# Performance work log

Hardware: AMD Instinct MI355X
Metric: run time of the kernel (lower is better)

The kernel has to match this reference:

```python
import jax, jax.numpy as jnp
import numpy as np

N_NODES = 100000


def _sage_conv(x, src, dst, W_l, W_r, b, num_nodes):
    # PyG SAGEConv with mean aggregation:
    # out_i = (mean_{j: (j->i) in E} x_j) @ W_l + x_i @ W_r + b
    msg_sum = jax.ops.segment_sum(x[src], dst, num_segments=num_nodes)  # [N, F]
    deg = jax.ops.segment_sum(jnp.ones_like(src, dtype=x.dtype), dst, num_segments=num_nodes)
    agg = msg_sum / jnp.maximum(deg, 1.0)[:, None]
    return agg @ W_l + x @ W_r + b


def setup_inputs() -> dict:
    key = jax.random.key(0)
    k = jax.random.split(key, 7)
    F_IN, H, C = 128, 128, 14
    E = 1600000
    x = jax.random.normal(k[0], (N_NODES, F_IN), dtype=jnp.float32)
    edge_index = jax.random.randint(k[1], (2, E), 0, N_NODES, dtype=jnp.int64)
    s = 1.0 / np.sqrt(F_IN)
    W1_l = jax.random.normal(k[2], (F_IN, H), dtype=jnp.float32) * s
    W1_r = jax.random.normal(k[3], (F_IN, H), dtype=jnp.float32) * s
    b1 = jnp.zeros((H,), dtype=jnp.float32)
    sh = 1.0 / np.sqrt(H)
    W2_l = jax.random.normal(k[4], (H, C), dtype=jnp.float32) * sh
    W2_r = jax.random.normal(k[5], (H, C), dtype=jnp.float32) * sh
    b2 = jnp.zeros((C,), dtype=jnp.float32)
    return {"x": x, "edge_index": edge_index, "edge_SF_num": 6,
            "W1_l": W1_l, "W1_r": W1_r, "b1": b1,
            "W2_l": W2_l, "W2_r": W2_r, "b2": b2}


def reference(x, edge_index, edge_SF_num, W1_l, W1_r, b1, W2_l, W2_r, b2):
    src, dst = edge_index[0], edge_index[1]
    h = _sage_conv(x, src, dst, W1_l, W1_r, b1, N_NODES)
    h = jax.nn.relu(h)
    # dropout is identity at inference (training=False)
    out = _sage_conv(h, src, dst, W2_l, W2_r, b2, N_NODES)
    x_SF = jax.nn.log_softmax(out[:, :edge_SF_num], axis=1)
    x_Ptx = jax.nn.log_softmax(out[:, edge_SF_num:], axis=1)
    return (x_SF, x_Ptx)
```

## Files before the change

kernel.cpp:

```cpp
#include <hip/hip_runtime.h>
#include <hip/hip_bf16.h>

#define NN 100000
#define F 128
#define C_OUT 14
#define ZP 16
#define WIN 64
#define NWIN ((NN + WIN - 1) / WIN)
#define WCAP 1408
#define EBATCH 4096
#define HS 136

typedef __attribute__((ext_vector_type(8))) short v8s;
typedef __attribute__((ext_vector_type(4))) float v4f;
typedef __attribute__((ext_vector_type(2))) float v2f;

static __device__ __forceinline__ unsigned short f2bf(float f) {
    unsigned int u = __float_as_uint(f);
    unsigned int r = (u + 0x7fffu + ((u >> 16) & 1u)) >> 16;
    return (unsigned short)r;
}
static __device__ __forceinline__ unsigned int pack2(float a, float b) {
    return (unsigned int)f2bf(a) | ((unsigned int)f2bf(b) << 16);
}
static __device__ __forceinline__ void unpack2(unsigned int u, float& lo, float& hi) {
    lo = __uint_as_float(u << 16);
    hi = __uint_as_float(u & 0xffff0000u);
}
static __device__ __forceinline__ void accf8(const uint2 u, float* a) {
    v2f f0 = __builtin_amdgcn_cvt_pk_f32_fp8((int)u.x, false);
    a[0] += f0[0]; a[1] += f0[1];
    v2f f1 = __builtin_amdgcn_cvt_pk_f32_fp8((int)u.x, true);
    a[2] += f1[0]; a[3] += f1[1];
    v2f f2 = __builtin_amdgcn_cvt_pk_f32_fp8((int)u.y, false);
    a[4] += f2[0]; a[5] += f2[1];
    v2f f3 = __builtin_amdgcn_cvt_pk_f32_fp8((int)u.y, true);
    a[6] += f3[0]; a[7] += f3[1];
}
static __device__ __forceinline__ unsigned int bf4_to_fp8x4(const unsigned short* sp) {
    float f0, f1, f2, f3;
    unpack2(*(const unsigned int*)(sp + 0), f0, f1);
    unpack2(*(const unsigned int*)(sp + 2), f2, f3);
    unsigned int w = __builtin_amdgcn_cvt_pk_fp8_f32(f0, f1, 0, false);
    return __builtin_amdgcn_cvt_pk_fp8_f32(f2, f3, w, true);
}

__global__ __launch_bounds__(256) void bin_kernel(
    const int* __restrict__ src, const int* __restrict__ dst,
    unsigned* __restrict__ bucket, int* __restrict__ wcur, int E)
{
    __shared__ int cnt_s[NWIN];
    __shared__ int gbase_s[NWIN];
    const int t = threadIdx.x;
    for (int w = t; w < NWIN; w += 256) cnt_s[w] = 0;
    __syncthreads();

    int      wreg[16];
    unsigned ereg[16];
    const int e0 = blockIdx.x * EBATCH;
    #pragma unroll
    for (int j = 0; j < 16; ++j) {
        const int e = e0 + j * 256 + t;
        int w = -1; unsigned ent = 0;
        if (e < E) {
            const int d = dst[e];
            const int s = src[e];
            w   = d >> 6;
            ent = ((unsigned)(d & (WIN - 1)) << 17) | (unsigned)s;
            atomicAdd(&cnt_s[w], 1);
        }
        wreg[j] = w; ereg[j] = ent;
    }
    __syncthreads();
    for (int w = t; w < NWIN; w += 256) {
        const int c = cnt_s[w];
        gbase_s[w] = c ? atomicAdd(&wcur[w], c) : 0;
    }
    __syncthreads();
    for (int w = t; w < NWIN; w += 256) cnt_s[w] = 0;
    __syncthreads();
    #pragma unroll
    for (int j = 0; j < 16; ++j) {
        const int w = wreg[j];
        if (w >= 0) {
            const int pos = gbase_s[w] + atomicAdd(&cnt_s[w], 1);
            if (pos < WCAP) bucket[(size_t)w * WCAP + pos] = ereg[j];
        }
    }
}

__global__ __launch_bounds__(256) void wprep_kernel(
    const float* __restrict__ W1l, const float* __restrict__ W1r,
    const float* __restrict__ W2l, const float* __restrict__ W2r,
    unsigned short* __restrict__ Wb, unsigned short* __restrict__ W2t)
{
    const int idx = blockIdx.x * 256 + threadIdx.x;
    if (idx < 2 * 128 * 128) {
        const int c   = idx >> 14;
        const int rem = idx & 16383;
        const int n   = rem >> 7;
        const int k   = rem & 127;
        const float* W = c ? W1r : W1l;
        Wb[idx] = f2bf(W[k * 128 + n]);
    } else if (idx < 2 * 128 * 128 + 32 * 128) {
        const int j = idx - 2 * 128 * 128;
        const int n = j >> 7;
        const int k = j & 127;
        float wv = 0.0f;
        if (n < 16) { if (n < C_OUT) wv = W2l[k * C_OUT + n]; }
        else        { if (n - 16 < C_OUT) wv = W2r[k * C_OUT + (n - 16)]; }
        W2t[j] = f2bf(wv);
    }
}

#define KSA 136
__global__ __launch_bounds__(256, 3) void pre1_kernel(
    const float* __restrict__ x, const unsigned short* __restrict__ Wb,
    const float* __restrict__ b1, unsigned char* __restrict__ pqa,
    unsigned short* __restrict__ pqs)
{
    __shared__ unsigned short A_s[64 * KSA];

    const int t    = threadIdx.x;
    const int m0   = blockIdx.x * 64;
    const int lane = t & 63;
    const int wave = t >> 6;
    const int lr   = lane & 15;
    const int quad = lane >> 4;
    const int nw0  = wave * 64;

    v8s bf[4][4];
    #pragma unroll
    for (int nt = 0; nt < 4; ++nt)
        #pragma unroll
        for (int ks = 0; ks < 4; ++ks)
            bf[nt][ks] = *(const v8s*)(Wb + (size_t)(nw0 + nt * 16 + lr) * 128 + ks * 32 + quad * 8);

    {
        const int mi = t & 63;
        const int ko = (t >> 6) * 32;
        const int m  = m0 + mi;
        unsigned short* dp = &A_s[mi * KSA + ko];
        if (m < NN) {
            const float4* sp = (const float4*)(x + (size_t)m * F + ko);
            #pragma unroll
            for (int j = 0; j < 8; j += 2) {
                const float4 f0 = sp[j], f1 = sp[j + 1];
                uint4 o;
                o.x = pack2(f0.x, f0.y); o.y = pack2(f0.z, f0.w);
                o.z = pack2(f1.x, f1.y); o.w = pack2(f1.z, f1.w);
                *(uint4*)(dp + j * 4) = o;
            }
        } else {
            #pragma unroll
            for (int j = 0; j < 4; ++j)
                *(uint4*)(dp + j * 8) = make_uint4(0u, 0u, 0u, 0u);
        }
    }
    __syncthreads();

    v4f acc[4][4];
    #pragma unroll
    for (int mt = 0; mt < 4; ++mt)
        #pragma unroll
        for (int nt = 0; nt < 4; ++nt)
            acc[mt][nt] = (v4f){0.f, 0.f, 0.f, 0.f};

    #pragma unroll
    for (int ks = 0; ks < 4; ++ks) {
        const int k0 = ks * 32 + quad * 8;
        #pragma unroll
        for (int mt = 0; mt < 4; ++mt) {
            const v8s a = *(const v8s*)&A_s[(mt * 16 + lr) * KSA + k0];
            acc[mt][0] = __builtin_amdgcn_mfma_f32_16x16x32_bf16(a, bf[0][ks], acc[mt][0], 0, 0, 0);
            acc[mt][1] = __builtin_amdgcn_mfma_f32_16x16x32_bf16(a, bf[1][ks], acc[mt][1], 0, 0, 0);
            acc[mt][2] = __builtin_amdgcn_mfma_f32_16x16x32_bf16(a, bf[2][ks], acc[mt][2], 0, 0, 0);
            acc[mt][3] = __builtin_amdgcn_mfma_f32_16x16x32_bf16(a, bf[3][ks], acc[mt][3], 0, 0, 0);
        }
    }
    __syncthreads();

    float bias[4];
    #pragma unroll
    for (int nt = 0; nt < 4; ++nt) {
        const int n = nw0 + nt * 16 + lr;
        bias[nt] = (n >= 128) ? b1[n - 128] : 0.0f;
    }

    unsigned short* C_s = A_s;
    #pragma unroll
    for (int p = 0; p < 2; ++p) {
        if ((nw0 >> 7) == p) {
            #pragma unroll
            for (int mt = 0; mt < 4; ++mt)
                #pragma unroll
                for (int nt = 0; nt < 4; ++nt) {
                    const int n = (nw0 & 127) + nt * 16 + lr;
                    #pragma unroll
                    for (int r = 0; r < 4; ++r) {
                        const int m = mt * 16 + quad * 4 + r;
                        C_s[m * KSA + n] = f2bf(acc[mt][nt][r] + bias[nt]);
                    }
                }
        }
        __syncthreads();
        if (p == 0) {
            const int mi8 = t >> 2;
            const int c0  = (t & 3) * 32;
            const int m   = m0 + mi8;
            if (m < NN) {
                unsigned char* dp = pqa + (size_t)m * 128 + c0;
                #pragma unroll
                for (int j = 0; j < 2; ++j) {
                    const unsigned short* sp = &C_s[mi8 * KSA + c0 + j * 16];
                    uint4 w;
                    w.x = bf4_to_fp8x4(sp + 0);
                    w.y = bf4_to_fp8x4(sp + 4);
                    w.z = bf4_to_fp8x4(sp + 8);
                    w.w = bf4_to_fp8x4(sp + 12);
                    *(uint4*)(dp + j * 16) = w;
                }
            }
        } else {
            const int mi = t >> 2;
            const int c0 = (t & 3) * 32;
            const int m  = m0 + mi;
            if (m < NN) {
                unsigned short* dp = pqs + (size_t)m * 128 + c0;
                const unsigned short* sp = &C_s[mi * KSA + c0];
                #pragma unroll
                for (int j = 0; j < 4; ++j)
                    *(uint4*)(dp + j * 8) = *(const uint4*)(sp + j * 8);
            }
        }
        __syncthreads();
    }
}

__global__ __launch_bounds__(256, 5) void agg1f_kernel(
    const unsigned char* __restrict__ pqa, const unsigned short* __restrict__ pqs,
    unsigned* __restrict__ bucket, const int* __restrict__ wcur,
    const unsigned short* __restrict__ W2t, const float* __restrict__ b2,
    int* __restrict__ wbase, unsigned short* __restrict__ z, float* __restrict__ r)
{
    __shared__ unsigned list[WCAP];
    __shared__ int cnt_s[WIN], base_s[WIN], cur_s[WIN];
    __shared__ unsigned short hsm[WIN * HS];
    __shared__ unsigned short W2s[32 * HS];
    const int t  = threadIdx.x;
    const int wb = blockIdx.x;
    const int cntw = min(wcur[wb], WCAP);
    unsigned* bp = bucket + (size_t)wb * WCAP;

    {
        const int row = t >> 3;
        const int c16 = (t & 7) * 16;
        *(uint4*)&W2s[row * HS + c16]     = *(const uint4*)&W2t[row * 128 + c16];
        *(uint4*)&W2s[row * HS + c16 + 8] = *(const uint4*)&W2t[row * 128 + c16 + 8];
    }

    if (t < WIN) cnt_s[t] = 0;
    __syncthreads();
    for (int i = t; i < cntw; i += 256) atomicAdd(&cnt_s[bp[i] >> 17], 1);
    __syncthreads();
    if (t < WIN) base_s[t] = cnt_s[t];
    __syncthreads();
    for (int off = 1; off < WIN; off <<= 1) {
        int v = 0;
        if (t < WIN && t >= off) v = base_s[t - off];
        __syncthreads();
        if (t < WIN) base_s[t] += v;
        __syncthreads();
    }
    if (t < WIN) { const int b = base_s[t] - cnt_s[t]; base_s[t] = b; cur_s[t] = b; }
    __syncthreads();
    for (int i = t; i < cntw; i += 256) {
        const unsigned e = bp[i];
        list[atomicAdd(&cur_s[e >> 17], 1)] = e & 0x1FFFFu;
    }
    __syncthreads();

    for (int i = t; i < cntw; i += 256) bp[i] = list[i];
    if (t < WIN) wbase[wb * WIN + t] = base_s[t];

    const int g    = t >> 4;
    const int lane = t & 15;
    const int col  = lane * 8;
    #pragma unroll
    for (int rep = 0; rep < 4; ++rep) {
        const int nloc = rep * 16 + g;
        const int n = wb * WIN + nloc;
        if (n >= NN) continue;
        const int start = base_s[nloc];
        const int len   = cnt_s[nloc];
        float a0[8] = {0,0,0,0,0,0,0,0};
        float a1[8] = {0,0,0,0,0,0,0,0};
        float a2[8] = {0,0,0,0,0,0,0,0};
        float a3[8] = {0,0,0,0,0,0,0,0};
        int i = 0;
        for (; i + 8 <= len; i += 8) {
            const int s0 = (int)list[start + i + 0];
            const int s1 = (int)list[start + i + 1];
            const int s2 = (int)list[start + i + 2];
            const int s3 = (int)list[start + i + 3];
            const int s4 = (int)list[start + i + 4];
            const int s5 = (int)list[start + i + 5];
            const int s6 = (int)list[start + i + 6];
            const int s7 = (int)list[start + i + 7];
            const uint2 u0 = *(const uint2*)(pqa + (size_t)s0 * 128 + col);
            const uint2 u1 = *(const uint2*)(pqa + (size_t)s1 * 128 + col);
            const uint2 u2 = *(const uint2*)(pqa + (size_t)s2 * 128 + col);
            const uint2 u3 = *(const uint2*)(pqa + (size_t)s3 * 128 + col);
            const uint2 u4 = *(const uint2*)(pqa + (size_t)s4 * 128 + col);
            const uint2 u5 = *(const uint2*)(pqa + (size_t)s5 * 128 + col);
            const uint2 u6 = *(const uint2*)(pqa + (size_t)s6 * 128 + col);
            const uint2 u7 = *(const uint2*)(pqa + (size_t)s7 * 128 + col);
            accf8(u0, a0); accf8(u1, a1); accf8(u2, a2); accf8(u3, a3);
            accf8(u4, a0); accf8(u5, a1); accf8(u6, a2); accf8(u7, a3);
        }
        for (; i + 4 <= len; i += 4) {
            const int s0 = (int)list[start + i + 0];
            const int s1 = (int)list[start + i + 1];
            const int s2 = (int)list[start + i + 2];
            const int s3 = (int)list[start + i + 3];
            const uint2 u0 = *(const uint2*)(pqa + (size_t)s0 * 128 + col);
            const uint2 u1 = *(const uint2*)(pqa + (size_t)s1 * 128 + col);
            const uint2 u2 = *(const uint2*)(pqa + (size_t)s2 * 128 + col);
            const uint2 u3 = *(const uint2*)(pqa + (size_t)s3 * 128 + col);
            accf8(u0, a0); accf8(u1, a1); accf8(u2, a2); accf8(u3, a3);
        }
        for (; i < len; ++i) {
            const int s = (int)list[start + i];
            const uint2 u = *(const uint2*)(pqa + (size_t)s * 128 + col);
            accf8(u, a0);
        }
        const float inv = 1.0f / (float)max(len, 1);
        const uint4 uq = *(const uint4*)(pqs + (size_t)n * 128 + col);
        float q[8];
        unpack2(uq.x, q[0], q[1]); unpack2(uq.y, q[2], q[3]);
        unpack2(uq.z, q[4], q[5]); unpack2(uq.w, q[6], q[7]);
        float hv[8];
        #pragma unroll
        for (int j = 0; j < 8; ++j)
            hv[j] = fmaxf((a0[j] + a1[j] + a2[j] + a3[j]) * inv + q[j], 0.0f);
        uint4 o;
        o.x = pack2(hv[0], hv[1]);
        o.y = pack2(hv[2], hv[3]);
        o.z = pack2(hv[4], hv[5]);
        o.w = pack2(hv[6], hv[7]);
        *(uint4*)&hsm[nloc * HS + col] = o;
    }
    __syncthreads();

    {
        const int wave = t >> 6;
        const int l64  = t & 63;
        const int lr   = l64 & 15;
        const int quad = l64 >> 4;
        const int m0w  = wave * 16;
        v4f accz = (v4f){0.f, 0.f, 0.f, 0.f};
        v4f accr = (v4f){0.f, 0.f, 0.f, 0.f};
        #pragma unroll
        for (int kt = 0; kt < 4; ++kt) {
            const int k0 = kt * 32 + quad * 8;
            const v8s a  = *(const v8s*)&hsm[(m0w + lr) * HS + k0];
            const v8s bz = *(const v8s*)&W2s[lr * HS + k0];
            const v8s br = *(const v8s*)&W2s[(16 + lr) * HS + k0];
            accz = __builtin_amdgcn_mfma_f32_16x16x32_bf16(a, bz, accz, 0, 0, 0);
            accr = __builtin_amdgcn_mfma_f32_16x16x32_bf16(a, br, accr, 0, 0, 0);
        }
        const float b2v = (lr < C_OUT) ? b2[lr] : 0.0f;
        #pragma unroll
        for (int rr = 0; rr < 4; ++rr) {
            const int m = m0w + quad * 4 + rr;
            const int n = wb * WIN + m;
            if (n < NN) {
                z[(size_t)n * ZP + lr] = f2bf(accz[rr]);
                r[(size_t)n * ZP + lr] = accr[rr] + b2v;
            }
        }
    }
}

__global__ __launch_bounds__(256) void agg2s_kernel(
    const unsigned short* __restrict__ z, const float* __restrict__ r,
    const unsigned* __restrict__ bucket, const int* __restrict__ wcur,
    const int* __restrict__ wbase, const int* __restrict__ sf_ptr,
    float* __restrict__ out)
{
    __shared__ unsigned list[WCAP];
    __shared__ int base_s[WIN + 1];
    __shared__ float sm[WIN][ZP + 1];
    const int t  = threadIdx.x;
    const int wb = blockIdx.x;
    const int cntw = min(wcur[wb], WCAP);
    const unsigned* bp = bucket + (size_t)wb * WCAP;

    if (t < WIN) base_s[t] = wbase[wb * WIN + t];
    if (t == 0) base_s[WIN] = cntw;
    for (int i = t; i < cntw; i += 256) list[i] = bp[i];
    __syncthreads();

    const int g  = t >> 2;
    const int j4 = (t & 3) * 4;
    const int n  = wb * WIN + g;
    if (n < NN) {
        const int start = base_s[g];
        const int len   = base_s[g + 1] - base_s[g];
        float4 a0 = make_float4(0.f, 0.f, 0.f, 0.f);
        float4 a1 = a0, a2 = a0, a3 = a0;
        int i = 0;
        for (; i + 8 <= len; i += 8) {
            const int s0 = (int)list[start + i + 0];
            const int s1 = (int)list[start + i + 1];
            const int s2 = (int)list[start + i + 2];
            const int s3 = (int)list[start + i + 3];
            const int s4 = (int)list[start + i + 4];
            const int s5 = (int)list[start + i + 5];
            const int s6 = (int)list[start + i + 6];
            const int s7 = (int)list[start + i + 7];
            const uint2 u0 = *(const uint2*)(z + (size_t)s0 * ZP + j4);
            const uint2 u1 = *(const uint2*)(z + (size_t)s1 * ZP + j4);
            const uint2 u2 = *(const uint2*)(z + (size_t)s2 * ZP + j4);
            const uint2 u3 = *(const uint2*)(z + (size_t)s3 * ZP + j4);
            const uint2 u4 = *(const uint2*)(z + (size_t)s4 * ZP + j4);
            const uint2 u5 = *(const uint2*)(z + (size_t)s5 * ZP + j4);
            const uint2 u6 = *(const uint2*)(z + (size_t)s6 * ZP + j4);
            const uint2 u7 = *(const uint2*)(z + (size_t)s7 * ZP + j4);
            float f0, f1, f2, f3;
            unpack2(u0.x, f0, f1); unpack2(u0.y, f2, f3);
            a0.x += f0; a0.y += f1; a0.z += f2; a0.w += f3;
            unpack2(u1.x, f0, f1); unpack2(u1.y, f2, f3);
            a1.x += f0; a1.y += f1; a1.z += f2; a1.w += f3;
            unpack2(u2.x, f0, f1); unpack2(u2.y, f2, f3);
            a2.x += f0; a2.y += f1; a2.z += f2; a2.w += f3;
            unpack2(u3.x, f0, f1); unpack2(u3.y, f2, f3);
            a3.x += f0; a3.y += f1; a3.z += f2; a3.w += f3;
            unpack2(u4.x, f0, f1); unpack2(u4.y, f2, f3);
            a0.x += f0; a0.y += f1; a0.z += f2; a0.w += f3;
            unpack2(u5.x, f0, f1); unpack2(u5.y, f2, f3);
            a1.x += f0; a1.y += f1; a1.z += f2; a1.w += f3;
            unpack2(u6.x, f0, f1); unpack2(u6.y, f2, f3);
            a2.x += f0; a2.y += f1; a2.z += f2; a2.w += f3;
            unpack2(u7.x, f0, f1); unpack2(u7.y, f2, f3);
            a3.x += f0; a3.y += f1; a3.z += f2; a3.w += f3;
        }
        for (; i + 4 <= len; i += 4) {
            const int s0 = (int)list[start + i + 0];
            const int s1 = (int)list[start + i + 1];
            const int s2 = (int)list[start + i + 2];
            const int s3 = (int)list[start + i + 3];
            const uint2 u0 = *(const uint2*)(z + (size_t)s0 * ZP + j4);
            const uint2 u1 = *(const uint2*)(z + (size_t)s1 * ZP + j4);
            const uint2 u2 = *(const uint2*)(z + (size_t)s2 * ZP + j4);
            const uint2 u3 = *(const uint2*)(z + (size_t)s3 * ZP + j4);
            float f0, f1, f2, f3;
            unpack2(u0.x, f0, f1); unpack2(u0.y, f2, f3);
            a0.x += f0; a0.y += f1; a0.z += f2; a0.w += f3;
            unpack2(u1.x, f0, f1); unpack2(u1.y, f2, f3);
            a1.x += f0; a1.y += f1; a1.z += f2; a1.w += f3;
            unpack2(u2.x, f0, f1); unpack2(u2.y, f2, f3);
            a2.x += f0; a2.y += f1; a2.z += f2; a2.w += f3;
            unpack2(u3.x, f0, f1); unpack2(u3.y, f2, f3);
            a3.x += f0; a3.y += f1; a3.z += f2; a3.w += f3;
        }
        for (; i < len; ++i) {
            const int s = (int)list[start + i];
            const uint2 u = *(const uint2*)(z + (size_t)s * ZP + j4);
            float f0, f1, f2, f3;
            unpack2(u.x, f0, f1); unpack2(u.y, f2, f3);
            a0.x += f0; a0.y += f1; a0.z += f2; a0.w += f3;
        }
        const float inv = 1.0f / (float)max(len, 1);
        const float4 rv = *(const float4*)(r + (size_t)n * ZP + j4);
        sm[g][j4 + 0] = (a0.x + a1.x + a2.x + a3.x) * inv + rv.x;
        sm[g][j4 + 1] = (a0.y + a1.y + a2.y + a3.y) * inv + rv.y;
        sm[g][j4 + 2] = (a0.z + a1.z + a2.z + a3.z) * inv + rv.z;
        sm[g][j4 + 3] = (a0.w + a1.w + a2.w + a3.w) * inv + rv.w;
    }
    __syncthreads();

    if (t < WIN) {
        const int n2 = wb * WIN + t;
        if (n2 < NN) {
            const int sf = *sf_ptr;
            const float* row = sm[t];
            float m = -1e30f;
            for (int c = 0; c < sf; ++c) m = fmaxf(m, row[c]);
            float s = 0.0f;
            for (int c = 0; c < sf; ++c) s += expf(row[c] - m);
            float ls = m + logf(s);
            for (int c = 0; c < sf; ++c)
                out[(long long)n2 * sf + c] = row[c] - ls;
            m = -1e30f;
            for (int c = sf; c < C_OUT; ++c) m = fmaxf(m, row[c]);
            s = 0.0f;
            for (int c = sf; c < C_OUT; ++c) s += expf(row[c] - m);
            ls = m + logf(s);
            const int pt = C_OUT - sf;
            for (int c = sf; c < C_OUT; ++c)
                out[(long long)NN * sf + (long long)n2 * pt + (c - sf)] = row[c] - ls;
        }
    }
}

extern "C" void kernel_launch(void* const* d_in, const int* in_sizes, int n_in,
                              void* d_out, int out_size, void* d_ws, size_t ws_size,
                              hipStream_t stream)
{
    const float* x   = (const float*)d_in[0];
    const int*   ei  = (const int*)d_in[1];
    const int*   sfp = (const int*)d_in[2];
    const float* W1l = (const float*)d_in[3];
    const float* W1r = (const float*)d_in[4];
    const float* b1  = (const float*)d_in[5];
    const float* W2l = (const float*)d_in[6];
    const float* W2r = (const float*)d_in[7];
    const float* b2  = (const float*)d_in[8];
    float*       out = (float*)d_out;

    const int E = in_sizes[1] / 2;
    const int* src = ei;
    const int* dst = ei + E;

    int*      wcur   = (int*)d_ws;
    int*      wbase  = wcur + 2048;
    unsigned* bucket = (unsigned*)(wbase + NWIN * WIN);
    unsigned short* Wb  = (unsigned short*)(bucket + (size_t)NWIN * WCAP);
    unsigned short* W2t = Wb + 2 * 128 * 128;
    unsigned short* pqs = W2t + 32 * 128;
    unsigned char*  pqa = (unsigned char*)(pqs + (size_t)NN * 128);
    unsigned short* z   = (unsigned short*)(pqa + (size_t)NN * 128);
    float*          r   = (float*)(z + (size_t)NN * ZP);

    hipMemsetAsync(wcur, 0, 2048 * sizeof(int), stream);

    bin_kernel<<<(E + EBATCH - 1) / EBATCH, 256, 0, stream>>>(src, dst, bucket, wcur, E);

    wprep_kernel<<<(2 * 128 * 128 + 32 * 128 + 255) / 256, 256, 0, stream>>>(
        W1l, W1r, W2l, W2r, Wb, W2t);

    pre1_kernel<<<(NN + 63) / 64, 256, 0, stream>>>(x, Wb, b1, pqa, pqs);

    agg1f_kernel<<<NWIN, 256, 0, stream>>>(pqa, pqs, bucket, wcur, W2t, b2, wbase, z, r);

    agg2s_kernel<<<NWIN, 256, 0, stream>>>(z, r, bucket, wcur, wbase, sfp, out);
}
```

Baseline: 219.0 us.

## Merge bin and weight-prep kernels; double-buffer gather loads in agg1f

Folds the weight conversion work into the edge binning launch as extra blocks, which removes one kernel launch. In the layer-1 aggregation, the 8-wide gather loop becomes software-pipelined with two register sets, so the next batch of fp8 row loads is issued before the current batch is accumulated. The occupancy hint drops from 5 to 4 blocks per CU to make room for the extra registers. The deeper memory-level parallelism may not make up for the lower occupancy.

```diff
diff --git a/kernel.cpp b/kernel.cpp
--- a/kernel.cpp
+++ b/kernel.cpp
@@ -10,6 +10,7 @@
 #define WCAP 1408
 #define EBATCH 4096
 #define HS 136
+#define WPREPB 144
 
 typedef __attribute__((ext_vector_type(8))) short v8s;
 typedef __attribute__((ext_vector_type(4))) float v4f;
@@ -45,13 +46,37 @@
     return __builtin_amdgcn_cvt_pk_fp8_f32(f2, f3, w, true);
 }
 
-__global__ __launch_bounds__(256) void bin_kernel(
+__global__ __launch_bounds__(256) void prep_kernel(
     const int* __restrict__ src, const int* __restrict__ dst,
-    unsigned* __restrict__ bucket, int* __restrict__ wcur, int E)
+    unsigned* __restrict__ bucket, int* __restrict__ wcur, int E, int binBlocks,
+    const float* __restrict__ W1l, const float* __restrict__ W1r,
+    const float* __restrict__ W2l, const float* __restrict__ W2r,
+    unsigned short* __restrict__ Wb, unsigned short* __restrict__ W2t)
 {
+    const int t = threadIdx.x;
+    if ((int)blockIdx.x >= binBlocks) {
+        const int idx = ((int)blockIdx.x - binBlocks) * 256 + t;
+        if (idx < 2 * 128 * 128) {
+            const int c   = idx >> 14;
+            const int rem = idx & 16383;
+            const int n   = rem >> 7;
+            const int k   = rem & 127;
+            const float* W = c ? W1r : W1l;
+            Wb[idx] = f2bf(W[k * 128 + n]);
+        } else if (idx < 2 * 128 * 128 + 32 * 128) {
+            const int j = idx - 2 * 128 * 128;
+            const int n = j >> 7;
+            const int k = j & 127;
+            float wv = 0.0f;
+            if (n < 16) { if (n < C_OUT) wv = W2l[k * C_OUT + n]; }
+            else        { if (n - 16 < C_OUT) wv = W2r[k * C_OUT + (n - 16)]; }
+            W2t[j] = f2bf(wv);
+        }
+        return;
+    }
+
     __shared__ int cnt_s[NWIN];
     __shared__ int gbase_s[NWIN];
-    const int t = threadIdx.x;
     for (int w = t; w < NWIN; w += 256) cnt_s[w] = 0;
     __syncthreads();
 
@@ -86,30 +111,6 @@
             const int pos = gbase_s[w] + atomicAdd(&cnt_s[w], 1);
             if (pos < WCAP) bucket[(size_t)w * WCAP + pos] = ereg[j];
         }
-    }
-}
-
-__global__ __launch_bounds__(256) void wprep_kernel(
-    const float* __restrict__ W1l, const float* __restrict__ W1r,
-    const float* __restrict__ W2l, const float* __restrict__ W2r,
-    unsigned short* __restrict__ Wb, unsigned short* __restrict__ W2t)
-{
-    const int idx = blockIdx.x * 256 + threadIdx.x;
-    if (idx < 2 * 128 * 128) {
-        const int c   = idx >> 14;
-        const int rem = idx & 16383;
-        const int n   = rem >> 7;
-        const int k   = rem & 127;
-        const float* W = c ? W1r : W1l;
-        Wb[idx] = f2bf(W[k * 128 + n]);
-    } else if (idx < 2 * 128 * 128 + 32 * 128) {
-        const int j = idx - 2 * 128 * 128;
-        const int n = j >> 7;
-        const int k = j & 127;
-        float wv = 0.0f;
-        if (n < 16) { if (n < C_OUT) wv = W2l[k * C_OUT + n]; }
-        else        { if (n - 16 < C_OUT) wv = W2r[k * C_OUT + (n - 16)]; }
-        W2t[j] = f2bf(wv);
     }
 }
 
@@ -237,7 +238,17 @@
     }
 }
 
-__global__ __launch_bounds__(256, 5) void agg1f_kernel(
+#define ISSUE8(U, B) { \
+    const int s0_=(int)lp[(B)+0], s1_=(int)lp[(B)+1], s2_=(int)lp[(B)+2], s3_=(int)lp[(B)+3], \
+              s4_=(int)lp[(B)+4], s5_=(int)lp[(B)+5], s6_=(int)lp[(B)+6], s7_=(int)lp[(B)+7]; \
+    U##0=*(const uint2*)(pqa+(size_t)s0_*128+col); U##1=*(const uint2*)(pqa+(size_t)s1_*128+col); \
+    U##2=*(const uint2*)(pqa+(size_t)s2_*128+col); U##3=*(const uint2*)(pqa+(size_t)s3_*128+col); \
+    U##4=*(const uint2*)(pqa+(size_t)s4_*128+col); U##5=*(const uint2*)(pqa+(size_t)s5_*128+col); \
+    U##6=*(const uint2*)(pqa+(size_t)s6_*128+col); U##7=*(const uint2*)(pqa+(size_t)s7_*128+col); }
+#define PROC8(U) { accf8(U##0,a0); accf8(U##1,a1); accf8(U##2,a2); accf8(U##3,a3); \
+                   accf8(U##4,a0); accf8(U##5,a1); accf8(U##6,a2); accf8(U##7,a3); }
+
+__global__ __launch_bounds__(256, 4) void agg1f_kernel(
     const unsigned char* __restrict__ pqa, const unsigned short* __restrict__ pqs,
     unsigned* __restrict__ bucket, const int* __restrict__ wcur,
     const unsigned short* __restrict__ W2t, const float* __restrict__ b2,
@@ -297,32 +308,31 @@
         float a1[8] = {0,0,0,0,0,0,0,0};
         float a2[8] = {0,0,0,0,0,0,0,0};
         float a3[8] = {0,0,0,0,0,0,0,0};
+        const unsigned* lp = list + start;
+        uint2 uA0,uA1,uA2,uA3,uA4,uA5,uA6,uA7;
+        uint2 uB0,uB1,uB2,uB3,uB4,uB5,uB6,uB7;
         int i = 0;
-        for (; i + 8 <= len; i += 8) {
-            const int s0 = (int)list[start + i + 0];
-            const int s1 = (int)list[start + i + 1];
-            const int s2 = (int)list[start + i + 2];
-            const int s3 = (int)list[start + i + 3];
-            const int s4 = (int)list[start + i + 4];
-            const int s5 = (int)list[start + i + 5];
-            const int s6 = (int)list[start + i + 6];
-            const int s7 = (int)list[start + i + 7];
-            const uint2 u0 = *(const uint2*)(pqa + (size_t)s0 * 128 + col);
-            const uint2 u1 = *(const uint2*)(pqa + (size_t)s1 * 128 + col);
-            const uint2 u2 = *(const uint2*)(pqa + (size_t)s2 * 128 + col);
-            const uint2 u3 = *(const uint2*)(pqa + (size_t)s3 * 128 + col);
-            const uint2 u4 = *(const uint2*)(pqa + (size_t)s4 * 128 + col);
-            const uint2 u5 = *(const uint2*)(pqa + (size_t)s5 * 128 + col);
-            const uint2 u6 = *(const uint2*)(pqa + (size_t)s6 * 128 + col);
-            const uint2 u7 = *(const uint2*)(pqa + (size_t)s7 * 128 + col);
-            accf8(u0, a0); accf8(u1, a1); accf8(u2, a2); accf8(u3, a3);
-            accf8(u4, a0); accf8(u5, a1); accf8(u6, a2); accf8(u7, a3);
+        if (len >= 8) ISSUE8(uA, 0);
+        for (; i + 24 <= len; i += 16) {
+            ISSUE8(uB, i + 8);
+            PROC8(uA);
+            ISSUE8(uA, i + 16);
+            PROC8(uB);
+        }
+        if (i + 16 <= len) {
+            ISSUE8(uB, i + 8);
+            PROC8(uA);
+            PROC8(uB);
+            i += 16;
+        } else if (i + 8 <= len) {
+            PROC8(uA);
+            i += 8;
         }
         for (; i + 4 <= len; i += 4) {
-            const int s0 = (int)list[start + i + 0];
-            const int s1 = (int)list[start + i + 1];
-            const int s2 = (int)list[start + i + 2];
-            const int s3 = (int)list[start + i + 3];
+            const int s0 = (int)lp[i + 0];
+            const int s1 = (int)lp[i + 1];
+            const int s2 = (int)lp[i + 2];
+            const int s3 = (int)lp[i + 3];
             const uint2 u0 = *(const uint2*)(pqa + (size_t)s0 * 128 + col);
             const uint2 u1 = *(const uint2*)(pqa + (size_t)s1 * 128 + col);
             const uint2 u2 = *(const uint2*)(pqa + (size_t)s2 * 128 + col);
@@ -330,12 +340,12 @@
             accf8(u0, a0); accf8(u1, a1); accf8(u2, a2); accf8(u3, a3);
         }
         for (; i < len; ++i) {
-            const int s = (int)list[start + i];
+            const int s = (int)lp[i];
             const uint2 u = *(const uint2*)(pqa + (size_t)s * 128 + col);
             accf8(u, a0);
         }
         const float inv = 1.0f / (float)max(len, 1);
-        const uint4 uq = *(const uint4*)(pqs + (size_t)n * 128 + col);
+        const uint4 uq = *(const uint4*)(pqs + (size_t)n * 128 + lane * 8);
         float q[8];
         unpack2(uq.x, q[0], q[1]); unpack2(uq.y, q[2], q[3]);
         unpack2(uq.z, q[4], q[5]); unpack2(uq.w, q[6], q[7]);
@@ -348,7 +358,7 @@
         o.y = pack2(hv[2], hv[3]);
         o.z = pack2(hv[4], hv[5]);
         o.w = pack2(hv[6], hv[7]);
-        *(uint4*)&hsm[nloc * HS + col] = o;
+        *(uint4*)&hsm[nloc * HS + lane * 8] = o;
     }
     __syncthreads();
 
@@ -535,10 +545,9 @@
 
     hipMemsetAsync(wcur, 0, 2048 * sizeof(int), stream);
 
-    bin_kernel<<<(E + EBATCH - 1) / EBATCH, 256, 0, stream>>>(src, dst, bucket, wcur, E);
-
-    wprep_kernel<<<(2 * 128 * 128 + 32 * 128 + 255) / 256, 256, 0, stream>>>(
-        W1l, W1r, W2l, W2r, Wb, W2t);
+    const int binBlocks = (E + EBATCH - 1) / EBATCH;
+    prep_kernel<<<binBlocks + WPREPB, 256, 0, stream>>>(
+        src, dst, bucket, wcur, E, binBlocks, W1l, W1r, W2l, W2r, Wb, W2t);
 
     pre1_kernel<<<(NN + 63) / 64, 256, 0, stream>>>(x, Wb, b1, pqa, pqs);
 
```

Measured after the change: 219.9 us. No clear change (+0.4%).
